# Kernel tuning notes

Measured on AMD Instinct MI355X. Metric: run time of the kernel, lower is better.

## Reference

```python
import jax, jax.numpy as jnp
import numpy as np

EPS = 0.5  # diffusion epsilon from init_kwargs

def setup_inputs() -> dict:
    key = jax.random.key(0)
    k = jax.random.split(key, 7)
    B, N0, N1, n = 1024, 32, 32, 64
    Mu0 = jax.random.normal(k[0], (N0, n), dtype=jnp.float32) * 2.0
    Mu1 = jax.random.normal(k[1], (N1, n), dtype=jnp.float32) * 2.0
    # diagonal covariances must be positive
    S0 = jax.random.uniform(k[2], (N0, n), dtype=jnp.float32, minval=0.1, maxval=1.0)
    S1 = jax.random.uniform(k[3], (N1, n), dtype=jnp.float32, minval=0.1, maxval=1.0)
    Lam = jax.random.uniform(k[4], (N0, N1), dtype=jnp.float32, minval=0.0, maxval=1.0)
    Lam = Lam / Lam.sum()  # transport plan sums to 1
    X = jax.random.normal(k[5], (B, n), dtype=jnp.float32)
    t = jnp.float32(0.3)
    return {"X": X, "Mu0": Mu0, "Mu1": Mu1, "S0": S0, "S1": S1, "Lam": Lam, "t": t}

def reference(X, Mu0, Mu1, S0, S1, Lam, t):
    eps2 = EPS * EPS
    S0e = S0[:, None, :]        # (N0,1,n)
    S1e = S1[None, :, :]        # (1,N1,n)
    Ds = jnp.sqrt(4.0 * S0e * S1e + EPS ** 4)
    Cs = 0.5 * (Ds - eps2)                       # (N0,N1,n)
    mu_t = (1.0 - t) * Mu0[:, None, :] + t * Mu1[None, :, :]  # (N0,N1,n)
    Sigma = (1.0 - t) ** 2 * S0e + t ** 2 * S1e + 2.0 * t * (1.0 - t) * (Cs + 0.5 * eps2)
    # St = Pt - Qt - eps^2 * t
    St = t * S1e + (1.0 - t) * Cs - ((1.0 - t) * S0e + t * Cs) - eps2 * t
    K = St / Sigma                               # (N0,N1,n)
    v = Mu1[None, :, :] - Mu0[:, None, :]        # (N0,N1,n)
    d = X[:, None, None, :] - mu_t               # (B,N0,N1,n)
    U = K * d + v                                # (B,N0,N1,n)
    # diag-Normal log_prob plus n/2*log(2pi) == -0.5*sum(d^2/Sigma + log Sigma)
    logw = -0.5 * jnp.sum(d * d / Sigma + jnp.log(Sigma), axis=-1)  # (B,N0,N1)
    W = jnp.exp(jnp.clip(logw, -50.0, 50.0)) * Lam                  # (B,N0,N1)
    num = jnp.einsum('bijn,bij->bn', U, W)       # (B,n)
    den = jnp.sum(W, axis=(1, 2))[:, None]       # (B,1)
    return num / den
```

## Files before the change

### kernel.cpp

```cpp
#include <hip/hip_runtime.h>
#include <math.h>

#define EPS2f 0.25f
#define EPS4f 0.0625f
#define BB 4

__global__ __launch_bounds__(256) void precomp_kernel(
    const float* __restrict__ Mu0, const float* __restrict__ Mu1,
    const float* __restrict__ S0,  const float* __restrict__ S1,
    const float* __restrict__ tptr,
    float2* __restrict__ AB4, float2* __restrict__ KV,
    float* __restrict__ C0)
{
    const int tid = threadIdx.x;
    const int k   = tid & 63;
    const int ij  = (blockIdx.x << 2) + (tid >> 6);
    const int i   = ij >> 5;
    const int j   = ij & 31;
    const float t   = *tptr;
    const float omt = 1.0f - t;

    const float s0 = S0[i * 64 + k];
    const float s1 = S1[j * 64 + k];
    const float m0 = Mu0[i * 64 + k];
    const float m1 = Mu1[j * 64 + k];

    const float ds  = sqrtf(4.0f * s0 * s1 + EPS4f);
    const float cs  = 0.5f * (ds - EPS2f);
    const float mt  = omt * m0 + t * m1;
    const float sig = omt * omt * s0 + t * t * s1
                    + 2.0f * t * omt * (cs + 0.5f * EPS2f);
    const float isig = 1.0f / sig;
    const float st = t * s1 - omt * s0 + (omt - t) * cs - EPS2f * t;
    const float kk = st * isig;
    const float v  = m1 - m0;

    AB4[((k >> 1) << 11) + (ij << 1) + (k & 1)] = make_float2(isig, 2.0f * mt * isig);
    KV[(ij << 6) + k] = make_float2(kk, v - kk * mt);

    float c = mt * mt * isig + __logf(sig);
    #pragma unroll
    for (int off = 32; off >= 1; off >>= 1)
        c += __shfl_xor(c, off, 64);
    if (k == 0) C0[ij] = c;
}

__global__ __launch_bounds__(1024, 4) void gmm_main_kernel(
    const float* __restrict__ X,   const float* __restrict__ Lam,
    const float* __restrict__ C0,
    const float4* __restrict__ AB4, const float2* __restrict__ KV,
    float* __restrict__ out)
{
    __shared__ float4 XsT[64];
    __shared__ float4 Wl[1024];
    __shared__ float  denp[16 * BB];
    __shared__ float  red[16 * 64 * 5];

    const int tid  = threadIdx.x;
    const int lane = tid & 63;
    const int w    = tid >> 6;
    const int b0   = blockIdx.x * BB;

    if (tid < 64 * BB) {
        ((float*)XsT)[(tid & 63) * BB + (tid >> 6)] = X[b0 * 64 + tid];
    }
    __syncthreads();

    const int ij = tid;
    float qa = 0.f, qb = 0.f, qc = 0.f, qd = 0.f;
    #pragma unroll 4
    for (int k2 = 0; k2 < 32; ++k2) {
        const float4 ab = AB4[(k2 << 10) + ij];
        const float4 x0 = XsT[2 * k2];
        const float4 x1 = XsT[2 * k2 + 1];
        qa = fmaf(fmaf(ab.x, x0.x, -ab.y), x0.x, qa);
        qb = fmaf(fmaf(ab.x, x0.y, -ab.y), x0.y, qb);
        qc = fmaf(fmaf(ab.x, x0.z, -ab.y), x0.z, qc);
        qd = fmaf(fmaf(ab.x, x0.w, -ab.y), x0.w, qd);
        qa = fmaf(fmaf(ab.z, x1.x, -ab.w), x1.x, qa);
        qb = fmaf(fmaf(ab.z, x1.y, -ab.w), x1.y, qb);
        qc = fmaf(fmaf(ab.z, x1.z, -ab.w), x1.z, qc);
        qd = fmaf(fmaf(ab.z, x1.w, -ab.w), x1.w, qd);
    }

    const float c0 = C0[ij], l0 = Lam[ij];
    #define WCALC(q) (__expf(fminf(fmaxf(-0.5f * ((q) + c0), -50.0f), 50.0f)) * l0)
    float4 wv4;
    wv4.x = WCALC(qa); wv4.y = WCALC(qb); wv4.z = WCALC(qc); wv4.w = WCALC(qd);
    #undef WCALC
    Wl[ij] = wv4;

    float d0 = wv4.x, d1 = wv4.y, d2 = wv4.z, d3 = wv4.w;
    #pragma unroll
    for (int off = 32; off >= 1; off >>= 1) {
        d0 += __shfl_xor(d0, off, 64);
        d1 += __shfl_xor(d1, off, 64);
        d2 += __shfl_xor(d2, off, 64);
        d3 += __shfl_xor(d3, off, 64);
    }
    if (lane == 0) {
        denp[w * BB + 0] = d0;
        denp[w * BB + 1] = d1;
        denp[w * BB + 2] = d2;
        denp[w * BB + 3] = d3;
    }

    const float4 xk4 = XsT[lane];
    float n0 = 0.f, n1 = 0.f, n2 = 0.f, n3 = 0.f;
    const int ijbase = w * 64;
    #pragma unroll 8
    for (int c = 0; c < 64; ++c) {
        const int ijb = ijbase + c;
        const float4 wv = Wl[ijb];
        const float2 kv = KV[(ijb << 6) + lane];
        float u;
        u = fmaf(kv.x, xk4.x, kv.y); n0 = fmaf(wv.x, u, n0);
        u = fmaf(kv.x, xk4.y, kv.y); n1 = fmaf(wv.y, u, n1);
        u = fmaf(kv.x, xk4.z, kv.y); n2 = fmaf(wv.z, u, n2);
        u = fmaf(kv.x, xk4.w, kv.y); n3 = fmaf(wv.w, u, n3);
    }
    {
        float* r = &red[(w * 64 + lane) * 5];
        r[0] = n0; r[1] = n1; r[2] = n2; r[3] = n3;
    }
    __syncthreads();

    if (tid < 256) {
        const int bb = tid >> 6;
        const int k  = tid & 63;
        float s = 0.f, d = 0.f;
        #pragma unroll
        for (int ww = 0; ww < 16; ++ww) {
            s += red[(ww * 64 + k) * 5 + bb];
            d += denp[ww * BB + bb];
        }
        out[b0 * 64 + tid] = s / d;
    }
}

extern "C" void kernel_launch(void* const* d_in, const int* in_sizes, int n_in,
                              void* d_out, int out_size, void* d_ws, size_t ws_size,
                              hipStream_t stream) {
    const float* X   = (const float*)d_in[0];
    const float* Mu0 = (const float*)d_in[1];
    const float* Mu1 = (const float*)d_in[2];
    const float* S0  = (const float*)d_in[3];
    const float* S1  = (const float*)d_in[4];
    const float* Lam = (const float*)d_in[5];
    const float* t   = (const float*)d_in[6];
    float* out = (float*)d_out;

    char* ws = (char*)d_ws;
    float2* AB4 = (float2*)(ws);
    float2* KV  = (float2*)(ws + (512 << 10));
    float*  C0  = (float*)(ws + (1024 << 10));

    precomp_kernel<<<256, 256, 0, stream>>>(Mu0, Mu1, S0, S1, t, AB4, KV, C0);
    gmm_main_kernel<<<256, 1024, 0, stream>>>(X, Lam, C0, (const float4*)AB4, KV, out);
}
```

Measured before the change: 80.87 us.

## Split mixture components across blocks with 16 batch rows per block and finalize pass

Each block now handles 16 batch rows against a quarter of the 1024 (i,j) components, not 4 rows against all components. This reuses each AB4/KV load across 16 rows instead of 4, cutting global traffic per output. The partial numerators and denominators are written to workspace and summed by a new finalize kernel. In exchange only 256 of 1024 threads do the quadratic-form phase, register use per thread grows, and there is an extra launch plus a partial-sum round trip.

```diff
diff --git a/kernel.cpp b/kernel.cpp
--- a/kernel.cpp
+++ b/kernel.cpp
@@ -3,7 +3,6 @@
 
 #define EPS2f 0.25f
 #define EPS4f 0.0625f
-#define BB 4
 
 __global__ __launch_bounds__(256) void precomp_kernel(
     const float* __restrict__ Mu0, const float* __restrict__ Mu1,
@@ -49,93 +48,130 @@
     const float* __restrict__ X,   const float* __restrict__ Lam,
     const float* __restrict__ C0,
     const float4* __restrict__ AB4, const float2* __restrict__ KV,
-    float* __restrict__ out)
+    float* __restrict__ pnum, float* __restrict__ pden)
 {
-    __shared__ float4 XsT[64];
-    __shared__ float4 Wl[1024];
-    __shared__ float  denp[16 * BB];
-    __shared__ float  red[16 * 64 * 5];
+    __shared__ float Xs[64 * 20];
+    __shared__ float XsT2[16 * 64];
+    __shared__ float Wl[256 * 20];
+    __shared__ float red[16 * 64 * 17];
 
     const int tid  = threadIdx.x;
     const int lane = tid & 63;
     const int w    = tid >> 6;
-    const int b0   = blockIdx.x * BB;
-
-    if (tid < 64 * BB) {
-        ((float*)XsT)[(tid & 63) * BB + (tid >> 6)] = X[b0 * 64 + tid];
+    const int q    = blockIdx.x & 3;
+    const int c    = blockIdx.x >> 2;
+
+    {
+        const int bb = w;
+        const float xv = X[(c * 16 + bb) * 64 + lane];
+        Xs[lane * 20 + bb]  = xv;
+        XsT2[bb * 64 + lane] = xv;
     }
     __syncthreads();
 
-    const int ij = tid;
-    float qa = 0.f, qb = 0.f, qc = 0.f, qd = 0.f;
+    if (tid < 256) {
+        const int ij_l = tid;
+        const int ij_g = (q << 8) + ij_l;
+        float acc[16];
+        #pragma unroll
+        for (int bb = 0; bb < 16; ++bb) acc[bb] = 0.f;
+
+        #pragma unroll 4
+        for (int k2 = 0; k2 < 32; ++k2) {
+            const float4 ab = AB4[(k2 << 10) + ij_g];
+            const float4* xr0 = (const float4*)&Xs[(2 * k2) * 20];
+            const float4* xr1 = (const float4*)&Xs[(2 * k2 + 1) * 20];
+            #pragma unroll
+            for (int g = 0; g < 4; ++g) {
+                const float4 x0 = xr0[g];
+                const float4 x1 = xr1[g];
+                acc[4*g+0] = fmaf(fmaf(ab.x, x0.x, -ab.y), x0.x, acc[4*g+0]);
+                acc[4*g+1] = fmaf(fmaf(ab.x, x0.y, -ab.y), x0.y, acc[4*g+1]);
+                acc[4*g+2] = fmaf(fmaf(ab.x, x0.z, -ab.y), x0.z, acc[4*g+2]);
+                acc[4*g+3] = fmaf(fmaf(ab.x, x0.w, -ab.y), x0.w, acc[4*g+3]);
+                acc[4*g+0] = fmaf(fmaf(ab.z, x1.x, -ab.w), x1.x, acc[4*g+0]);
+                acc[4*g+1] = fmaf(fmaf(ab.z, x1.y, -ab.w), x1.y, acc[4*g+1]);
+                acc[4*g+2] = fmaf(fmaf(ab.z, x1.z, -ab.w), x1.z, acc[4*g+2]);
+                acc[4*g+3] = fmaf(fmaf(ab.z, x1.w, -ab.w), x1.w, acc[4*g+3]);
+            }
+        }
+
+        const float c0v = C0[ij_g];
+        const float lm  = Lam[ij_g];
+        float4* wrow = (float4*)&Wl[ij_l * 20];
+        #pragma unroll
+        for (int g = 0; g < 4; ++g) {
+            float4 wv;
+            wv.x = __expf(fminf(fmaxf(-0.5f * (acc[4*g+0] + c0v), -50.0f), 50.0f)) * lm;
+            wv.y = __expf(fminf(fmaxf(-0.5f * (acc[4*g+1] + c0v), -50.0f), 50.0f)) * lm;
+            wv.z = __expf(fminf(fmaxf(-0.5f * (acc[4*g+2] + c0v), -50.0f), 50.0f)) * lm;
+            wv.w = __expf(fminf(fmaxf(-0.5f * (acc[4*g+3] + c0v), -50.0f), 50.0f)) * lm;
+            wrow[g] = wv;
+        }
+    }
+    __syncthreads();
+
+    float xk[16];
+    #pragma unroll
+    for (int bb = 0; bb < 16; ++bb) xk[bb] = XsT2[bb * 64 + lane];
+    float n[16];
+    #pragma unroll
+    for (int bb = 0; bb < 16; ++bb) n[bb] = 0.f;
+
+    const int ijb0 = w << 4;
     #pragma unroll 4
-    for (int k2 = 0; k2 < 32; ++k2) {
-        const float4 ab = AB4[(k2 << 10) + ij];
-        const float4 x0 = XsT[2 * k2];
-        const float4 x1 = XsT[2 * k2 + 1];
-        qa = fmaf(fmaf(ab.x, x0.x, -ab.y), x0.x, qa);
-        qb = fmaf(fmaf(ab.x, x0.y, -ab.y), x0.y, qb);
-        qc = fmaf(fmaf(ab.x, x0.z, -ab.y), x0.z, qc);
-        qd = fmaf(fmaf(ab.x, x0.w, -ab.y), x0.w, qd);
-        qa = fmaf(fmaf(ab.z, x1.x, -ab.w), x1.x, qa);
-        qb = fmaf(fmaf(ab.z, x1.y, -ab.w), x1.y, qb);
-        qc = fmaf(fmaf(ab.z, x1.z, -ab.w), x1.z, qc);
-        qd = fmaf(fmaf(ab.z, x1.w, -ab.w), x1.w, qd);
-    }
-
-    const float c0 = C0[ij], l0 = Lam[ij];
-    #define WCALC(q) (__expf(fminf(fmaxf(-0.5f * ((q) + c0), -50.0f), 50.0f)) * l0)
-    float4 wv4;
-    wv4.x = WCALC(qa); wv4.y = WCALC(qb); wv4.z = WCALC(qc); wv4.w = WCALC(qd);
-    #undef WCALC
-    Wl[ij] = wv4;
-
-    float d0 = wv4.x, d1 = wv4.y, d2 = wv4.z, d3 = wv4.w;
-    #pragma unroll
-    for (int off = 32; off >= 1; off >>= 1) {
-        d0 += __shfl_xor(d0, off, 64);
-        d1 += __shfl_xor(d1, off, 64);
-        d2 += __shfl_xor(d2, off, 64);
-        d3 += __shfl_xor(d3, off, 64);
-    }
-    if (lane == 0) {
-        denp[w * BB + 0] = d0;
-        denp[w * BB + 1] = d1;
-        denp[w * BB + 2] = d2;
-        denp[w * BB + 3] = d3;
-    }
-
-    const float4 xk4 = XsT[lane];
-    float n0 = 0.f, n1 = 0.f, n2 = 0.f, n3 = 0.f;
-    const int ijbase = w * 64;
-    #pragma unroll 8
-    for (int c = 0; c < 64; ++c) {
-        const int ijb = ijbase + c;
-        const float4 wv = Wl[ijb];
-        const float2 kv = KV[(ijb << 6) + lane];
-        float u;
-        u = fmaf(kv.x, xk4.x, kv.y); n0 = fmaf(wv.x, u, n0);
-        u = fmaf(kv.x, xk4.y, kv.y); n1 = fmaf(wv.y, u, n1);
-        u = fmaf(kv.x, xk4.z, kv.y); n2 = fmaf(wv.z, u, n2);
-        u = fmaf(kv.x, xk4.w, kv.y); n3 = fmaf(wv.w, u, n3);
-    }
+    for (int cc = 0; cc < 16; ++cc) {
+        const int ij_l = ijb0 + cc;
+        const float2 kv = KV[(((q << 8) + ij_l) << 6) + lane];
+        const float4* wrow = (const float4*)&Wl[ij_l * 20];
+        #pragma unroll
+        for (int g = 0; g < 4; ++g) {
+            const float4 wv = wrow[g];
+            float u;
+            u = fmaf(kv.x, xk[4*g+0], kv.y); n[4*g+0] = fmaf(wv.x, u, n[4*g+0]);
+            u = fmaf(kv.x, xk[4*g+1], kv.y); n[4*g+1] = fmaf(wv.y, u, n[4*g+1]);
+            u = fmaf(kv.x, xk[4*g+2], kv.y); n[4*g+2] = fmaf(wv.z, u, n[4*g+2]);
+            u = fmaf(kv.x, xk[4*g+3], kv.y); n[4*g+3] = fmaf(wv.w, u, n[4*g+3]);
+        }
+    }
+    #pragma unroll
+    for (int bb = 0; bb < 16; ++bb)
+        red[(w * 64 + lane) * 17 + bb] = n[bb];
+    __syncthreads();
+
     {
-        float* r = &red[(w * 64 + lane) * 5];
-        r[0] = n0; r[1] = n1; r[2] = n2; r[3] = n3;
-    }
-    __syncthreads();
-
-    if (tid < 256) {
-        const int bb = tid >> 6;
-        const int k  = tid & 63;
-        float s = 0.f, d = 0.f;
-        #pragma unroll
-        for (int ww = 0; ww < 16; ++ww) {
-            s += red[(ww * 64 + k) * 5 + bb];
-            d += denp[ww * BB + bb];
-        }
-        out[b0 * 64 + tid] = s / d;
-    }
+        const int bb = w;
+        float s = 0.f;
+        #pragma unroll
+        for (int ww = 0; ww < 16; ++ww)
+            s += red[(ww * 64 + lane) * 17 + bb];
+        pnum[((((q << 6) + c) << 4) + bb) * 64 + lane] = s;
+
+        float d = Wl[lane * 20 + bb]        + Wl[(lane + 64) * 20 + bb]
+                + Wl[(lane + 128) * 20 + bb] + Wl[(lane + 192) * 20 + bb];
+        #pragma unroll
+        for (int off = 32; off >= 1; off >>= 1)
+            d += __shfl_xor(d, off, 64);
+        if (lane == 0) pden[((q << 6) + c) * 16 + bb] = d;
+    }
+}
+
+__global__ __launch_bounds__(1024) void finalize_kernel(
+    const float* __restrict__ pnum, const float* __restrict__ pden,
+    float* __restrict__ out)
+{
+    const int idx = blockIdx.x * 1024 + threadIdx.x;
+    const int k   = idx & 63;
+    const int b   = idx >> 6;
+    const int c   = b >> 4;
+    const int bb  = b & 15;
+    float s = 0.f, d = 0.f;
+    #pragma unroll
+    for (int qq = 0; qq < 4; ++qq) {
+        s += pnum[((((qq << 6) + c) << 4) + bb) * 64 + k];
+        d += pden[((qq << 6) + c) * 16 + bb];
+    }
+    out[idx] = s / d;
 }
 
 extern "C" void kernel_launch(void* const* d_in, const int* in_sizes, int n_in,
@@ -154,7 +190,11 @@
     float2* AB4 = (float2*)(ws);
     float2* KV  = (float2*)(ws + (512 << 10));
     float*  C0  = (float*)(ws + (1024 << 10));
+    float*  pden = (float*)(ws + (1024 << 10) + (16 << 10));
+    float*  pnum = (float*)(ws + (1024 << 10) + (64 << 10));
 
     precomp_kernel<<<256, 256, 0, stream>>>(Mu0, Mu1, S0, S1, t, AB4, KV, C0);
-    gmm_main_kernel<<<256, 1024, 0, stream>>>(X, Lam, C0, (const float4*)AB4, KV, out);
-}
+    gmm_main_kernel<<<256, 1024, 0, stream>>>(X, Lam, C0, (const float4*)AB4, KV,
+                                              pnum, pden);
+    finalize_kernel<<<64, 1024, 0, stream>>>(pnum, pden, out);
+}
```

New measurement: 92.06 us. 1.14x slower.
